# Kernel tuning notes

Hardware: AMD Instinct MI355X
Metric: run time of the kernel (lower is better)

The kernel has to match this reference:

```python
import jax, jax.numpy as jnp
import numpy as np

B, S, D, H, L = 2, 4096, 768, 12, 2
DH = D // H
W = 256            # one-sided sliding window (longformer-base attention_window=512)
VOCAB = 50265
SEP_ID = 2
N_SEPS = 63
G = N_SEPS + 1     # global tokens: <s> at pos 0 + all </s> separators
FF = 4 * D
C = 7
NEG = -1e9


def layer_norm(x, s, b, eps=1e-5):
    m = x.mean(-1, keepdims=True)
    v = ((x - m) ** 2).mean(-1, keepdims=True)
    return (x - m) * jax.lax.rsqrt(v + eps) * s + b


def setup_inputs():
    key = jax.random.key(0)
    keys = iter(jax.random.split(key, 64))
    def nrm(shape, sd=0.02):
        return jax.random.normal(next(keys), shape, jnp.float32) * sd
    input_ids = jax.random.randint(next(keys), (B, S), 5, VOCAB, dtype=jnp.int32)
    input_ids = input_ids.at[:, 0].set(0)  # <s>
    sep_pos = (jnp.arange(N_SEPS) + 1) * (S // (N_SEPS + 1))  # 64,128,...,4032
    input_ids = input_ids.at[:, sep_pos].set(SEP_ID)
    return dict(
        emb_tok=nrm((VOCAB, D)), emb_pos=nrm((S, D)),
        ln_e_s=jnp.ones((D,)), ln_e_b=jnp.zeros((D,)),
        Wq=nrm((L, D, D)), bq=jnp.zeros((L, D)),
        Wk=nrm((L, D, D)), bk=jnp.zeros((L, D)),
        Wv=nrm((L, D, D)), bv=jnp.zeros((L, D)),
        Wqg=nrm((L, D, D)), bqg=jnp.zeros((L, D)),
        Wkg=nrm((L, D, D)), bkg=jnp.zeros((L, D)),
        Wvg=nrm((L, D, D)), bvg=jnp.zeros((L, D)),
        Wo=nrm((L, D, D)), bo=jnp.zeros((L, D)),
        ln1_s=jnp.ones((L, D)), ln1_b=jnp.zeros((L, D)),
        Wf1=nrm((L, D, FF)), bf1=jnp.zeros((L, FF)),
        Wf2=nrm((L, FF, D)), bf2=jnp.zeros((L, D)),
        ln2_s=jnp.ones((L, D)), ln2_b=jnp.zeros((L, D)),
        Wc=nrm((D, C)), bc=jnp.zeros((C,)),
        input_ids=input_ids,
        attention_mask=jnp.ones((B, S), jnp.int32),
        left_overlap=2, right_overlap=2,
    )


def _forward(emb_tok, emb_pos, ln_e_s, ln_e_b, Wq, bq, Wk, bk, Wv, bv,
             Wqg, bqg, Wkg, bkg, Wvg, bvg, Wo, bo, ln1_s, ln1_b,
             Wf1, bf1, Wf2, bf2, ln2_s, ln2_b, Wc, bc,
             input_ids, attention_mask, left_overlap, right_overlap):
    pos = jnp.arange(S)
    # global attention mask: first token + every </s> token (as in the torch forward)
    g_mask = (input_ids == SEP_ID) | (pos[None, :] == 0)                         # [B,S]
    idx_g = jax.vmap(lambda m: jnp.nonzero(m, size=G, fill_value=0)[0])(g_mask)  # [B,G]
    am = attention_mask.astype(jnp.float32)
    key_local_ok = am * (1.0 - g_mask.astype(jnp.float32))  # globals excluded from windowed keys
    nb = S // W
    band_idx = jnp.arange(nb)[:, None] * W + jnp.arange(3 * W)[None, :]  # [nb,3W] into W-padded seq
    rel = jnp.arange(3 * W)[None, :] - W - jnp.arange(W)[:, None]        # key_pos - query_pos
    band_ok = (jnp.abs(rel) <= W)[None, None, None]                       # [1,1,1,W,3W]
    kv_ok = jnp.pad(key_local_ok, ((0, 0), (W, W)))[:, band_idx] > 0      # [B,nb,3W]
    mask = band_ok & kv_ok[:, None, :, None, :]                           # [B,1,nb,W,3W]
    scale = float(DH) ** -0.5
    bix = jnp.arange(B)[:, None]

    x = emb_tok[input_ids] + emb_pos[None]
    x = layer_norm(x, ln_e_s, ln_e_b)
    for l in range(L):
        q = (x @ Wq[l] + bq[l]).reshape(B, S, H, DH)
        k = (x @ Wk[l] + bk[l]).reshape(B, S, H, DH)
        v = (x @ Wv[l] + bv[l]).reshape(B, S, H, DH)
        kb = jnp.pad(k, ((0, 0), (W, W), (0, 0), (0, 0)))[:, band_idx]    # [B,nb,3W,H,DH]
        vb = jnp.pad(v, ((0, 0), (W, W), (0, 0), (0, 0)))[:, band_idx]
        s_band = jnp.einsum('bnqhd,bnkhd->bhnqk', q.reshape(B, nb, W, H, DH), kb) * scale
        s_band = jnp.where(mask, s_band, NEG)
        kg = jnp.take_along_axis(k, idx_g[:, :, None, None], axis=1)      # [B,G,H,DH]
        vg = jnp.take_along_axis(v, idx_g[:, :, None, None], axis=1)
        s_glob = jnp.einsum('bqhd,bghd->bhqg', q, kg) * scale
        probs = jax.nn.softmax(
            jnp.concatenate([s_band.reshape(B, H, S, 3 * W), s_glob], axis=-1), axis=-1)
        out = (jnp.einsum('bhnqk,bnkhd->bnqhd',
                          probs[..., :3 * W].reshape(B, H, nb, W, 3 * W), vb).reshape(B, S, H, DH)
               + jnp.einsum('bhqg,bghd->bqhd', probs[..., 3 * W:], vg)).reshape(B, S, D)
        # global query rows: full attention over all tokens with dedicated global projections
        xg = jnp.take_along_axis(x, idx_g[:, :, None], axis=1)            # [B,G,D]
        qg = (xg @ Wqg[l] + bqg[l]).reshape(B, G, H, DH)
        kga = (x @ Wkg[l] + bkg[l]).reshape(B, S, H, DH)
        vga = (x @ Wvg[l] + bvg[l]).reshape(B, S, H, DH)
        sg = jnp.where(am[:, None, None, :] > 0,
                       jnp.einsum('bghd,bshd->bhgs', qg, kga) * scale, NEG)
        og = jnp.einsum('bhgs,bshd->bghd', jax.nn.softmax(sg, axis=-1), vga).reshape(B, G, D)
        out = out.at[bix, idx_g].set(og)
        x = layer_norm(x + out @ Wo[l] + bo[l], ln1_s[l], ln1_b[l])
        x = layer_norm(x + jax.nn.gelu(x @ Wf1[l] + bf1[l]) @ Wf2[l] + bf2[l], ln2_s[l], ln2_b[l])
    # classification head (eval-mode dropout = identity). Faithful to the torch code,
    # which gathers hidden states at token POSITION j for j in [left, n_seps - right).
    core = x[:, left_overlap:N_SEPS - right_overlap, :]                    # [B, n_core, D]
    return (core @ Wc + bc).reshape(-1, C)


def reference(emb_tok, emb_pos, ln_e_s, ln_e_b, Wq, bq, Wk, bk, Wv, bv,
              Wqg, bqg, Wkg, bkg, Wvg, bvg, Wo, bo, ln1_s, ln1_b,
              Wf1, bf1, Wf2, bf2, ln2_s, ln2_b, Wc, bc,
              input_ids, attention_mask, left_overlap, right_overlap):
    return _forward(emb_tok, emb_pos, ln_e_s, ln_e_b, Wq, bq, Wk, bk, Wv, bv,
                    Wqg, bqg, Wkg, bkg, Wvg, bvg, Wo, bo, ln1_s, ln1_b,
                    Wf1, bf1, Wf2, bf2, ln2_s, ln2_b, Wc, bc,
                    input_ids, attention_mask, left_overlap, right_overlap)
```

## Files before the change

### kernel.cpp

```cpp
#include <hip/hip_runtime.h>
#include <hip/hip_bf16.h>
#include <stdint.h>

#define B_ 2
#define S_ 4096
#define D_ 768
#define H_ 12
#define DH_ 64
#define L_ 2
#define W_ 256
#define G_ 64
#define FF_ 3072
#define C_ 7
#define SEP_ 2
#define NEG_ (-1000000000.0f)
#define NC_ 16

typedef __attribute__((ext_vector_type(8))) short short8;
typedef __attribute__((ext_vector_type(4))) float f32x4;

__device__ __forceinline__ float bfu2f(unsigned short u) {
    return __uint_as_float(((unsigned int)u) << 16);
}
__device__ __forceinline__ unsigned short f2bfu(float f) {
    unsigned int x = __float_as_uint(f);
    unsigned int r = (x + 0x7fffu + ((x >> 16) & 1u)) >> 16;
    return (unsigned short)r;
}
__device__ __forceinline__ float gelu_tanh(float v) {
    float c = 0.7978845608028654f * (v + 0.044715f * v * v * v);
    return 0.5f * v * (1.0f + tanhf(c));
}

__global__ __launch_bounds__(256) void k_wtrans(
    const float* __restrict__ src, unsigned short* __restrict__ dst,
    int K, int N, size_t dstStride) {
    int l = blockIdx.z;
    src += (size_t)l * K * N;
    dst += (size_t)l * dstStride;
    __shared__ unsigned short tile[32][36];
    int t = threadIdx.x;
    int r = t >> 3, c4 = (t & 7) << 2;
    int k0 = blockIdx.y << 5, n0 = blockIdx.x << 5;
    float4 v = *(const float4*)(src + (size_t)(k0 + r) * N + n0 + c4);
    tile[c4 + 0][r] = f2bfu(v.x);
    tile[c4 + 1][r] = f2bfu(v.y);
    tile[c4 + 2][r] = f2bfu(v.z);
    tile[c4 + 3][r] = f2bfu(v.w);
    __syncthreads();
    ushort4 o;
    o.x = tile[r][c4 + 0]; o.y = tile[r][c4 + 1];
    o.z = tile[r][c4 + 2]; o.w = tile[r][c4 + 3];
    *(ushort4*)(dst + (size_t)(n0 + r) * K + k0 + c4) = o;
}

__global__ __launch_bounds__(256) void k_embed_ln(
    const int* __restrict__ ids, const float* __restrict__ etok,
    const float* __restrict__ epos, const float* __restrict__ lns,
    const float* __restrict__ lnb, float* __restrict__ x,
    unsigned short* __restrict__ xb) {
    int row = (blockIdx.x << 2) + (threadIdx.x >> 6);
    int lane = threadIdx.x & 63;
    int s = row & (S_ - 1);
    int id = ids[row];
    const float4* ep = (const float4*)(etok + (size_t)id * D_);
    const float4* pp = (const float4*)(epos + (size_t)s * D_);
    float4 a[3];
    float sum = 0.f, sum2 = 0.f;
#pragma unroll
    for (int i = 0; i < 3; i++) {
        float4 ev = ep[lane + i * 64];
        float4 pv = pp[lane + i * 64];
        ev.x += pv.x; ev.y += pv.y; ev.z += pv.z; ev.w += pv.w;
        a[i] = ev;
        sum  += ev.x + ev.y + ev.z + ev.w;
        sum2 += ev.x * ev.x + ev.y * ev.y + ev.z * ev.z + ev.w * ev.w;
    }
#pragma unroll
    for (int off = 1; off < 64; off <<= 1) {
        sum += __shfl_xor(sum, off);
        sum2 += __shfl_xor(sum2, off);
    }
    float mean = sum * (1.0f / D_);
    float var = sum2 * (1.0f / D_) - mean * mean;
    float rs = rsqrtf(var + 1e-5f);
    float4* xp = (float4*)(x + (size_t)row * D_);
#pragma unroll
    for (int i = 0; i < 3; i++) {
        float4 g = *(const float4*)(lns + lane * 4 + i * 256);
        float4 bb = *(const float4*)(lnb + lane * 4 + i * 256);
        float4 v;
        v.x = (a[i].x - mean) * rs * g.x + bb.x;
        v.y = (a[i].y - mean) * rs * g.y + bb.y;
        v.z = (a[i].z - mean) * rs * g.z + bb.z;
        v.w = (a[i].w - mean) * rs * g.w + bb.w;
        xp[lane + i * 64] = v;
        ushort4 u; u.x = f2bfu(v.x); u.y = f2bfu(v.y); u.z = f2bfu(v.z); u.w = f2bfu(v.w);
        *(ushort4*)(xb + (size_t)row * D_ + lane * 4 + i * 256) = u;
    }
}

__global__ __launch_bounds__(256) void k_add_ln(
    float* __restrict__ x, const float* __restrict__ y, const float* __restrict__ y2,
    const float* __restrict__ lns, const float* __restrict__ lnb,
    unsigned short* __restrict__ xb) {
    int row = (blockIdx.x << 2) + (threadIdx.x >> 6);
    int lane = threadIdx.x & 63;
    float4* xp = (float4*)(x + (size_t)row * D_);
    const float4* yp = (const float4*)(y + (size_t)row * D_);
    const float4* y2p = y2 ? (const float4*)(y2 + (size_t)row * D_) : nullptr;
    float4 a[3];
    float sum = 0.f, sum2 = 0.f;
#pragma unroll
    for (int i = 0; i < 3; i++) {
        float4 xv = xp[lane + i * 64];
        float4 yv = yp[lane + i * 64];
        xv.x += yv.x; xv.y += yv.y; xv.z += yv.z; xv.w += yv.w;
        if (y2p) {
            float4 zv = y2p[lane + i * 64];
            xv.x += zv.x; xv.y += zv.y; xv.z += zv.z; xv.w += zv.w;
        }
        a[i] = xv;
        sum  += xv.x + xv.y + xv.z + xv.w;
        sum2 += xv.x * xv.x + xv.y * xv.y + xv.z * xv.z + xv.w * xv.w;
    }
#pragma unroll
    for (int off = 1; off < 64; off <<= 1) {
        sum += __shfl_xor(sum, off);
        sum2 += __shfl_xor(sum2, off);
    }
    float mean = sum * (1.0f / D_);
    float var = sum2 * (1.0f / D_) - mean * mean;
    float rs = rsqrtf(var + 1e-5f);
#pragma unroll
    for (int i = 0; i < 3; i++) {
        float4 g = *(const float4*)(lns + lane * 4 + i * 256);
        float4 bb = *(const float4*)(lnb + lane * 4 + i * 256);
        float4 v;
        v.x = (a[i].x - mean) * rs * g.x + bb.x;
        v.y = (a[i].y - mean) * rs * g.y + bb.y;
        v.z = (a[i].z - mean) * rs * g.z + bb.z;
        v.w = (a[i].w - mean) * rs * g.w + bb.w;
        xp[lane + i * 64] = v;
        ushort4 u; u.x = f2bfu(v.x); u.y = f2bfu(v.y); u.z = f2bfu(v.z); u.w = f2bfu(v.w);
        *(ushort4*)(xb + (size_t)row * D_ + lane * 4 + i * 256) = u;
    }
}

__global__ __launch_bounds__(256) void k_idx(const int* __restrict__ ids, int* __restrict__ idxg) {
    int b = blockIdx.x;
    int t = threadIdx.x;
    __shared__ int cnt[256];
    __shared__ int totsh;
    int loc[16];
    int n = 0;
#pragma unroll
    for (int i = 0; i < 16; i++) {
        int s = t * 16 + i;
        if (s == 0 || ids[b * S_ + s] == SEP_) loc[n++] = s;
    }
    cnt[t] = n;
    __syncthreads();
    int base = 0;
    for (int u = 0; u < t; u++) base += cnt[u];
    for (int i = 0; i < n; i++) {
        int o = base + i;
        if (o < G_) idxg[b * G_ + o] = loc[i];
    }
    if (t == 255) totsh = base + n;
    __syncthreads();
    if (t == 0)
        for (int o = totsh; o < G_; o++) idxg[b * G_ + o] = 0;
}

__global__ __launch_bounds__(256) void k_gemm_mfma(
    const unsigned short* __restrict__ A, const unsigned short* __restrict__ Wt,
    const float* __restrict__ Wf, const float* __restrict__ bias,
    float* __restrict__ Cf, float* __restrict__ Cf2, unsigned short* __restrict__ Cb,
    int M, int N, int K, int act) {
    __shared__ unsigned short As[128][40];
    __shared__ unsigned short Bs[128][40];
    int t = threadIdx.x;
    int wave = t >> 6, lane = t & 63, l16 = lane & 15, quad = lane >> 4;
    int m0 = blockIdx.y << 7, n0 = blockIdx.x << 7;
    int wm = (wave >> 1) << 6, wn = (wave & 1) << 6;
    int slice = blockIdx.z;
    int kper = K / gridDim.z;
    int kbeg = slice * kper, kend = kbeg + kper;
    f32x4 acc[4][4];
#pragma unroll
    for (int i = 0; i < 4; i++)
#pragma unroll
        for (int j = 0; j < 4; j++) acc[i][j] = (f32x4){0.f, 0.f, 0.f, 0.f};

    int ar = t >> 1, akc = (t & 1) << 4;
    int bn = t & 127, bkh = (t >> 7) << 4;

    for (int k0 = kbeg; k0 < kend; k0 += 32) {
        const unsigned short* ap = A + (size_t)(m0 + ar) * K + k0 + akc;
        *(uint4*)&As[ar][akc] = *(const uint4*)ap;
        *(uint4*)&As[ar][akc + 8] = *(const uint4*)(ap + 8);
        if (Wt) {
            const unsigned short* bp = Wt + (size_t)(n0 + bn) * K + k0 + bkh;
            *(uint4*)&Bs[bn][bkh] = *(const uint4*)bp;
            *(uint4*)&Bs[bn][bkh + 8] = *(const uint4*)(bp + 8);
        } else {
            const float* bp = Wf + (size_t)(k0 + bkh) * N + n0 + bn;
            unsigned int pk[8];
#pragma unroll
            for (int i = 0; i < 8; i++) {
                unsigned int lo = f2bfu(bp[(size_t)(2 * i) * N]);
                unsigned int hi = f2bfu(bp[(size_t)(2 * i + 1) * N]);
                pk[i] = lo | (hi << 16);
            }
            *(uint4*)&Bs[bn][bkh] = *(uint4*)&pk[0];
            *(uint4*)&Bs[bn][bkh + 8] = *(uint4*)&pk[4];
        }
        __syncthreads();
        short8 af[4], bf[4];
#pragma unroll
        for (int i = 0; i < 4; i++) af[i] = *(const short8*)&As[wm + i * 16 + l16][quad * 8];
#pragma unroll
        for (int j = 0; j < 4; j++) bf[j] = *(const short8*)&Bs[wn + j * 16 + l16][quad * 8];
#pragma unroll
        for (int i = 0; i < 4; i++)
#pragma unroll
            for (int j = 0; j < 4; j++)
                acc[i][j] = __builtin_amdgcn_mfma_f32_16x16x32_bf16(af[i], bf[j], acc[i][j], 0, 0, 0);
        __syncthreads();
    }
    float bj[4];
#pragma unroll
    for (int j = 0; j < 4; j++) bj[j] = (slice == 0) ? bias[n0 + wn + j * 16 + l16] : 0.f;
    float* outp = (slice == 0) ? Cf : Cf2;
#pragma unroll
    for (int i = 0; i < 4; i++)
#pragma unroll
        for (int j = 0; j < 4; j++) {
            int col = n0 + wn + j * 16 + l16;
#pragma unroll
            for (int r = 0; r < 4; r++) {
                int row = m0 + wm + i * 16 + quad * 4 + r;
                float v = acc[i][j][r] + bj[j];
                if (act) v = gelu_tanh(v);
                if (outp) outp[(size_t)row * N + col] = v;
                else      Cb[(size_t)row * N + col] = f2bfu(v);
            }
        }
}

struct P5 {
    const unsigned short* Wt[5];
    const float* Wf[5];
    const float* bias[5];
    unsigned short* out[5];
};
__global__ __launch_bounds__(256) void k_gemm_qkv5(
    const unsigned short* __restrict__ A, P5 p) {
    __shared__ unsigned short As[128][40];
    __shared__ unsigned short Bs[128][40];
    const unsigned short* __restrict__ Wt = p.Wt[blockIdx.z];
    const float* __restrict__ Wf = p.Wf[blockIdx.z];
    const float* __restrict__ bias = p.bias[blockIdx.z];
    unsigned short* __restrict__ Cb = p.out[blockIdx.z];
    const int N = D_, K = D_;
    int t = threadIdx.x;
    int wave = t >> 6, lane = t & 63, l16 = lane & 15, quad = lane >> 4;
    int m0 = blockIdx.y << 7, n0 = blockIdx.x << 7;
    int wm = (wave >> 1) << 6, wn = (wave & 1) << 6;
    f32x4 acc[4][4];
#pragma unroll
    for (int i = 0; i < 4; i++)
#pragma unroll
        for (int j = 0; j < 4; j++) acc[i][j] = (f32x4){0.f, 0.f, 0.f, 0.f};

    int ar = t >> 1, akc = (t & 1) << 4;
    int bn = t & 127, bkh = (t >> 7) << 4;

    for (int k0 = 0; k0 < K; k0 += 32) {
        const unsigned short* ap = A + (size_t)(m0 + ar) * K + k0 + akc;
        *(uint4*)&As[ar][akc] = *(const uint4*)ap;
        *(uint4*)&As[ar][akc + 8] = *(const uint4*)(ap + 8);
        if (Wt) {
            const unsigned short* bp = Wt + (size_t)(n0 + bn) * K + k0 + bkh;
            *(uint4*)&Bs[bn][bkh] = *(const uint4*)bp;
            *(uint4*)&Bs[bn][bkh + 8] = *(const uint4*)(bp + 8);
        } else {
            const float* bp = Wf + (size_t)(k0 + bkh) * N + n0 + bn;
            unsigned int pk[8];
#pragma unroll
            for (int i = 0; i < 8; i++) {
                unsigned int lo = f2bfu(bp[(size_t)(2 * i) * N]);
                unsigned int hi = f2bfu(bp[(size_t)(2 * i + 1) * N]);
                pk[i] = lo | (hi << 16);
            }
            *(uint4*)&Bs[bn][bkh] = *(uint4*)&pk[0];
            *(uint4*)&Bs[bn][bkh + 8] = *(uint4*)&pk[4];
        }
        __syncthreads();
        short8 af[4], bf[4];
#pragma unroll
        for (int i = 0; i < 4; i++) af[i] = *(const short8*)&As[wm + i * 16 + l16][quad * 8];
#pragma unroll
        for (int j = 0; j < 4; j++) bf[j] = *(const short8*)&Bs[wn + j * 16 + l16][quad * 8];
#pragma unroll
        for (int i = 0; i < 4; i++)
#pragma unroll
            for (int j = 0; j < 4; j++)
                acc[i][j] = __builtin_amdgcn_mfma_f32_16x16x32_bf16(af[i], bf[j], acc[i][j], 0, 0, 0);
        __syncthreads();
    }
    float bj[4];
#pragma unroll
    for (int j = 0; j < 4; j++) bj[j] = bias[n0 + wn + j * 16 + l16];
#pragma unroll
    for (int i = 0; i < 4; i++)
#pragma unroll
        for (int j = 0; j < 4; j++) {
            int col = n0 + wn + j * 16 + l16;
#pragma unroll
            for (int r = 0; r < 4; r++) {
                int row = m0 + wm + i * 16 + quad * 4 + r;
                float v = acc[i][j][r] + bj[j];
                size_t adr = ((((size_t)(row >> 12)) * H_ + (col >> 6)) * S_ +
                              (row & (S_ - 1))) * DH_ + (col & 63);
                Cb[adr] = f2bfu(v);
            }
        }
}

__global__ __launch_bounds__(256) void k_lattn(
    const unsigned short* __restrict__ q, const unsigned short* __restrict__ k,
    const unsigned short* __restrict__ v, const int* __restrict__ ids,
    const int* __restrict__ am, const int* __restrict__ idxg,
    unsigned short* __restrict__ Tb) {
    int s0 = blockIdx.x << 6, h = blockIdx.y, b = blockIdx.z;
    int t = threadIdx.x;
    int wave = t >> 6, lane = t & 63, l16 = lane & 15, quad = lane >> 4;

    __shared__ unsigned short Ks[64][72];
    __shared__ unsigned short Vt[64][72];
    __shared__ unsigned short Ps[64][72];
    __shared__ unsigned char keyok[64];

    const size_t headbase = (((size_t)b * H_) + h) * S_;
    int qrow = s0 + wave * 16 + l16;
    const unsigned short* qptr = q + (headbase + qrow) * DH_;
    short8 qa0 = *(const short8*)(qptr + quad * 8);
    short8 qa1 = *(const short8*)(qptr + 32 + quad * 8);

    f32x4 O[4];
#pragma unroll
    for (int nf = 0; nf < 4; nf++) O[nf] = (f32x4){0.f, 0.f, 0.f, 0.f};
    float m_run[4] = {-3.4e38f, -3.4e38f, -3.4e38f, -3.4e38f};
    float l_run[4] = {0.f, 0.f, 0.f, 0.f};

    int kbase = s0 - 256;
    int sr = t >> 2, sc = t & 3;

    for (int tile = 0; tile < 10; tile++) {
        int sK, sclamp; bool okf;
        if (tile < 9) {
            sK = kbase + tile * 64 + sr;
            bool inr = (sK >= 0) && (sK < S_);
            sclamp = inr ? sK : 0;
            okf = inr && (am[b * S_ + sclamp] != 0) &&
                  !((ids[b * S_ + sclamp] == SEP_) || (sK == 0));
        } else {
            sK = idxg[b * G_ + sr];
            sclamp = sK; okf = true;
        }
        if (sc == 0) keyok[sr] = okf ? 1 : 0;
        const unsigned short* srcK = k + (headbase + sclamp) * DH_;
        const unsigned short* srcV = v + (headbase + sclamp) * DH_;
        uint4 k0v = *(const uint4*)(srcK + sc * 8);
        uint4 k1v = *(const uint4*)(srcK + (sc + 4) * 8);
        uint4 v0v = *(const uint4*)(srcV + sc * 8);
        uint4 v1v = *(const uint4*)(srcV + (sc + 4) * 8);
        *(uint4*)&Ks[sr][sc * 8] = k0v;
        *(uint4*)&Ks[sr][(sc + 4) * 8] = k1v;
        const unsigned int* vw0 = (const unsigned int*)&v0v;
        const unsigned int* vw1 = (const unsigned int*)&v1v;
#pragma unroll
        for (int i = 0; i < 4; i++) {
            Vt[sc * 8 + 2 * i][sr]      = (unsigned short)(vw0[i] & 0xffff);
            Vt[sc * 8 + 2 * i + 1][sr]  = (unsigned short)(vw0[i] >> 16);
            Vt[(sc + 4) * 8 + 2 * i][sr]     = (unsigned short)(vw1[i] & 0xffff);
            Vt[(sc + 4) * 8 + 2 * i + 1][sr] = (unsigned short)(vw1[i] >> 16);
        }
        __syncthreads();

        f32x4 Sf[4];
#pragma unroll
        for (int nf = 0; nf < 4; nf++) {
            short8 b0 = *(const short8*)&Ks[nf * 16 + l16][quad * 8];
            short8 b1 = *(const short8*)&Ks[nf * 16 + l16][32 + quad * 8];
            f32x4 a = (f32x4){0.f, 0.f, 0.f, 0.f};
            a = __builtin_amdgcn_mfma_f32_16x16x32_bf16(qa0, b0, a, 0, 0, 0);
            a = __builtin_amdgcn_mfma_f32_16x16x32_bf16(qa1, b1, a, 0, 0, 0);
            Sf[nf] = a;
        }
        int ktb = kbase + tile * 64;
        bool kval[4];
#pragma unroll
        for (int nf = 0; nf < 4; nf++) kval[nf] = (tile == 9) || (keyok[nf * 16 + l16] != 0);
        float P_[4][4];
        float mt[4];
#pragma unroll
        for (int r = 0; r < 4; r++) {
            int qs = s0 + wave * 16 + quad * 4 + r;
            float mx = -3.4e38f;
#pragma unroll
            for (int nf = 0; nf < 4; nf++) {
                int ks2 = ktb + nf * 16 + l16;
                bool ok = kval[nf] && ((tile == 9) || (ks2 >= qs - 256 && ks2 <= qs + 256));
                float sv = ok ? Sf[nf][r] * 0.125f : NEG_;
                P_[nf][r] = sv;
                mx = fmaxf(mx, sv);
            }
            mt[r] = mx;
        }
#pragma unroll
        for (int off = 1; off < 16; off <<= 1)
#pragma unroll
            for (int r = 0; r < 4; r++) mt[r] = fmaxf(mt[r], __shfl_xor(mt[r], off));
        float alpha[4], lt[4];
#pragma unroll
        for (int r = 0; r < 4; r++) {
            float mn = fmaxf(m_run[r], mt[r]);
            alpha[r] = __expf(m_run[r] - mn);
            m_run[r] = mn; lt[r] = 0.f;
        }
#pragma unroll
        for (int nf = 0; nf < 4; nf++)
#pragma unroll
            for (int r = 0; r < 4; r++) {
                float p = (P_[nf][r] > -1.0e8f) ? __expf(P_[nf][r] - m_run[r]) : 0.f;
                P_[nf][r] = p; lt[r] += p;
            }
#pragma unroll
        for (int off = 1; off < 16; off <<= 1)
#pragma unroll
            for (int r = 0; r < 4; r++) lt[r] += __shfl_xor(lt[r], off);
#pragma unroll
        for (int r = 0; r < 4; r++) l_run[r] = l_run[r] * alpha[r] + lt[r];
#pragma unroll
        for (int nf = 0; nf < 4; nf++) {
            O[nf][0] *= alpha[0]; O[nf][1] *= alpha[1];
            O[nf][2] *= alpha[2]; O[nf][3] *= alpha[3];
        }
#pragma unroll
        for (int nf = 0; nf < 4; nf++)
#pragma unroll
            for (int r = 0; r < 4; r++)
                Ps[wave * 16 + quad * 4 + r][nf * 16 + l16] = f2bfu(P_[nf][r]);
#pragma unroll
        for (int hh = 0; hh < 2; hh++) {
            short8 pa = *(const short8*)&Ps[wave * 16 + l16][hh * 32 + quad * 8];
#pragma unroll
            for (int nf = 0; nf < 4; nf++) {
                short8 vb8 = *(const short8*)&Vt[nf * 16 + l16][hh * 32 + quad * 8];
                O[nf] = __builtin_amdgcn_mfma_f32_16x16x32_bf16(pa, vb8, O[nf], 0, 0, 0);
            }
        }
        __syncthreads();
    }
#pragma unroll
    for (int r = 0; r < 4; r++) {
        int qs = s0 + wave * 16 + quad * 4 + r;
        float invl = 1.0f / l_run[r];
        size_t base = ((size_t)(b * S_ + qs)) * D_ + h * DH_;
#pragma unroll
        for (int nf = 0; nf < 4; nf++)
            Tb[base + nf * 16 + l16] = f2bfu(O[nf][r] * invl);
    }
}

__global__ __launch_bounds__(256) void k_gattn_part(
    const unsigned short* __restrict__ qg, const unsigned short* __restrict__ kga,
    const unsigned short* __restrict__ vga, const int* __restrict__ am,
    float* __restrict__ Opart, float* __restrict__ mbuf, float* __restrict__ lbuf) {
    int c = blockIdx.x, h = blockIdx.y, b = blockIdx.z;
    int t = threadIdx.x;
    int wave = t >> 6, lane = t & 63, l16 = lane & 15, quad = lane >> 4;

    __shared__ unsigned short Ks[64][72];
    __shared__ unsigned short Vt[64][72];
    __shared__ unsigned short Ps[64][72];
    __shared__ unsigned char keyok[64];

    const size_t headbase = (((size_t)b * H_) + h) * S_;
    int grow = wave * 16 + l16;
    const unsigned short* qptr = qg + ((size_t)(b * G_ + grow)) * D_ + h * DH_;
    short8 qa0 = *(const short8*)(qptr + quad * 8);
    short8 qa1 = *(const short8*)(qptr + 32 + quad * 8);

    f32x4 O[4];
#pragma unroll
    for (int nf = 0; nf < 4; nf++) O[nf] = (f32x4){0.f, 0.f, 0.f, 0.f};
    float m_run[4] = {-3.4e38f, -3.4e38f, -3.4e38f, -3.4e38f};
    float l_run[4] = {0.f, 0.f, 0.f, 0.f};

    int kbase = c * 256;
    int sr = t >> 2, sc = t & 3;

    for (int tile = 0; tile < 4; tile++) {
        int sK = kbase + tile * 64 + sr;
        if (sc == 0) keyok[sr] = (am[b * S_ + sK] != 0) ? 1 : 0;
        const unsigned short* srcK = kga + (headbase + sK) * DH_;
        const unsigned short* srcV = vga + (headbase + sK) * DH_;
        uint4 k0v = *(const uint4*)(srcK + sc * 8);
        uint4 k1v = *(const uint4*)(srcK + (sc + 4) * 8);
        uint4 v0v = *(const uint4*)(srcV + sc * 8);
        uint4 v1v = *(const uint4*)(srcV + (sc + 4) * 8);
        *(uint4*)&Ks[sr][sc * 8] = k0v;
        *(uint4*)&Ks[sr][(sc + 4) * 8] = k1v;
        const unsigned int* vw0 = (const unsigned int*)&v0v;
        const unsigned int* vw1 = (const unsigned int*)&v1v;
#pragma unroll
        for (int i = 0; i < 4; i++) {
            Vt[sc * 8 + 2 * i][sr]      = (unsigned short)(vw0[i] & 0xffff);
            Vt[sc * 8 + 2 * i + 1][sr]  = (unsigned short)(vw0[i] >> 16);
            Vt[(sc + 4) * 8 + 2 * i][sr]     = (unsigned short)(vw1[i] & 0xffff);
            Vt[(sc + 4) * 8 + 2 * i + 1][sr] = (unsigned short)(vw1[i] >> 16);
        }
        __syncthreads();

        f32x4 Sf[4];
#pragma unroll
        for (int nf = 0; nf < 4; nf++) {
            short8 b0 = *(const short8*)&Ks[nf * 16 + l16][quad * 8];
            short8 b1 = *(const short8*)&Ks[nf * 16 + l16][32 + quad * 8];
            f32x4 a = (f32x4){0.f, 0.f, 0.f, 0.f};
            a = __builtin_amdgcn_mfma_f32_16x16x32_bf16(qa0, b0, a, 0, 0, 0);
            a = __builtin_amdgcn_mfma_f32_16x16x32_bf16(qa1, b1, a, 0, 0, 0);
            Sf[nf] = a;
        }
        bool kval[4];
#pragma unroll
        for (int nf = 0; nf < 4; nf++) kval[nf] = (keyok[nf * 16 + l16] != 0);
        float P_[4][4];
        float mt[4];
#pragma unroll
        for (int r = 0; r < 4; r++) {
            float mx = -3.4e38f;
#pragma unroll
            for (int nf = 0; nf < 4; nf++) {
                float sv = kval[nf] ? Sf[nf][r] * 0.125f : NEG_;
                P_[nf][r] = sv;
                mx = fmaxf(mx, sv);
            }
            mt[r] = mx;
        }
#pragma unroll
        for (int off = 1; off < 16; off <<= 1)
#pragma unroll
            for (int r = 0; r < 4; r++) mt[r] = fmaxf(mt[r], __shfl_xor(mt[r], off));
        float alpha[4], lt[4];
#pragma unroll
        for (int r = 0; r < 4; r++) {
            float mn = fmaxf(m_run[r], mt[r]);
            alpha[r] = __expf(m_run[r] - mn);
            m_run[r] = mn; lt[r] = 0.f;
        }
#pragma unroll
        for (int nf = 0; nf < 4; nf++)
#pragma unroll
            for (int r = 0; r < 4; r++) {
                float p = (P_[nf][r] > -1.0e8f) ? __expf(P_[nf][r] - m_run[r]) : 0.f;
                P_[nf][r] = p; lt[r] += p;
            }
#pragma unroll
        for (int off = 1; off < 16; off <<= 1)
#pragma unroll
            for (int r = 0; r < 4; r++) lt[r] += __shfl_xor(lt[r], off);
#pragma unroll
        for (int r = 0; r < 4; r++) l_run[r] = l_run[r] * alpha[r] + lt[r];
#pragma unroll
        for (int nf = 0; nf < 4; nf++) {
            O[nf][0] *= alpha[0]; O[nf][1] *= alpha[1];
            O[nf][2] *= alpha[2]; O[nf][3] *= alpha[3];
        }
#pragma unroll
        for (int nf = 0; nf < 4; nf++)
#pragma unroll
            for (int r = 0; r < 4; r++)
                Ps[wave * 16 + quad * 4 + r][nf * 16 + l16] = f2bfu(P_[nf][r]);
#pragma unroll
        for (int hh = 0; hh < 2; hh++) {
            short8 pa = *(const short8*)&Ps[wave * 16 + l16][hh * 32 + quad * 8];
#pragma unroll
            for (int nf = 0; nf < 4; nf++) {
                short8 vb8 = *(const short8*)&Vt[nf * 16 + l16][hh * 32 + quad * 8];
                O[nf] = __builtin_amdgcn_mfma_f32_16x16x32_bf16(pa, vb8, O[nf], 0, 0, 0);
            }
        }
        __syncthreads();
    }
    size_t bhc = ((size_t)(b * H_ + h)) * NC_ + c;
#pragma unroll
    for (int r = 0; r < 4; r++) {
        int row = wave * 16 + quad * 4 + r;
#pragma unroll
        for (int nf = 0; nf < 4; nf++)
            Opart[bhc * (G_ * DH_) + (size_t)row * DH_ + nf * 16 + l16] = O[nf][r];
        if (l16 == 0) {
            mbuf[bhc * G_ + row] = m_run[r];
            lbuf[bhc * G_ + row] = l_run[r];
        }
    }
}

__global__ __launch_bounds__(64) void k_gattn_comb(
    const float* __restrict__ Opart, const float* __restrict__ mbuf,
    const float* __restrict__ lbuf, const int* __restrict__ idxg,
    unsigned short* __restrict__ Tb) {
    int g = blockIdx.x, h = blockIdx.y, b = blockIdx.z;
    int d = threadIdx.x;
    size_t bh = (size_t)(b * H_ + h);
    float M = -3.4e38f;
    float mv[NC_];
#pragma unroll
    for (int c = 0; c < NC_; c++) {
        mv[c] = mbuf[(bh * NC_ + c) * G_ + g];
        M = fmaxf(M, mv[c]);
    }
    float L = 0.f, o = 0.f;
#pragma unroll
    for (int c = 0; c < NC_; c++) {
        float e = __expf(mv[c] - M);
        L += lbuf[(bh * NC_ + c) * G_ + g] * e;
        o += Opart[(bh * NC_ + c) * (G_ * DH_) + (size_t)g * DH_ + d] * e;
    }
    int srow = idxg[b * G_ + g];
    Tb[((size_t)(b * S_ + srow)) * D_ + h * DH_ + d] = f2bfu(o / L);
}

__global__ __launch_bounds__(256) void k_gemm(
    const float* __restrict__ A, const float* __restrict__ Bw,
    const float* __restrict__ bias, float* __restrict__ Cf,
    unsigned short* __restrict__ Cb, int M, int N, int K, int act) {
    __shared__ float As[16][68];
    __shared__ float Bs[16][68];
    int tl = threadIdx.x;
    int tx = tl & 15, ty = tl >> 4;
    int m0 = blockIdx.y << 6, n0 = blockIdx.x << 6;
    float c[4][4] = {{0.f}};
    int arow = tl >> 2, akk = (tl & 3) << 2;
    int bkk = tl >> 4, bcol = (tl & 15) << 2;
    for (int k0 = 0; k0 < K; k0 += 16) {
        float4 a4 = *(const float4*)(A + (size_t)(m0 + arow) * K + k0 + akk);
        As[akk + 0][arow] = a4.x; As[akk + 1][arow] = a4.y;
        As[akk + 2][arow] = a4.z; As[akk + 3][arow] = a4.w;
        float4 b4 = *(const float4*)(Bw + (size_t)(k0 + bkk) * N + n0 + bcol);
        Bs[bkk][bcol + 0] = b4.x; Bs[bkk][bcol + 1] = b4.y;
        Bs[bkk][bcol + 2] = b4.z; Bs[bkk][bcol + 3] = b4.w;
        __syncthreads();
#pragma unroll
        for (int kk = 0; kk < 16; kk++) {
            float4 av = *(const float4*)&As[kk][ty << 2];
            float4 bv = *(const float4*)&Bs[kk][tx << 2];
            float aa[4] = {av.x, av.y, av.z, av.w};
            float bb[4] = {bv.x, bv.y, bv.z, bv.w};
#pragma unroll
            for (int i = 0; i < 4; i++)
#pragma unroll
                for (int j = 0; j < 4; j++) c[i][j] += aa[i] * bb[j];
        }
        __syncthreads();
    }
    float bias4[4];
#pragma unroll
    for (int j = 0; j < 4; j++) bias4[j] = bias[n0 + (tx << 2) + j];
#pragma unroll
    for (int i = 0; i < 4; i++) {
        int mrow = m0 + (ty << 2) + i;
        float v0 = c[i][0] + bias4[0], v1 = c[i][1] + bias4[1];
        float v2 = c[i][2] + bias4[2], v3 = c[i][3] + bias4[3];
        if (act) { v0 = gelu_tanh(v0); v1 = gelu_tanh(v1); v2 = gelu_tanh(v2); v3 = gelu_tanh(v3); }
        if (Cf) {
            float4 o; o.x = v0; o.y = v1; o.z = v2; o.w = v3;
            *(float4*)(Cf + (size_t)mrow * N + n0 + (tx << 2)) = o;
        } else {
            ushort4 o; o.x = f2bfu(v0); o.y = f2bfu(v1); o.z = f2bfu(v2); o.w = f2bfu(v3);
            *(ushort4*)(Cb + (size_t)mrow * N + n0 + (tx << 2)) = o;
        }
    }
}

__global__ __launch_bounds__(256) void k_gather_xg(
    const float* __restrict__ x, const int* __restrict__ idxg, float* __restrict__ xg) {
    int bg = blockIdx.x;
    int b = bg / G_;
    int srow = idxg[bg];
    for (int d = threadIdx.x; d < D_; d += 256)
        xg[(size_t)bg * D_ + d] = x[((size_t)(b * S_ + srow)) * D_ + d];
}

__global__ __launch_bounds__(256) void k_classifier(
    const float* __restrict__ x, const float* __restrict__ Wc,
    const float* __restrict__ bc, const int* __restrict__ lo_p,
    int rows_pb, float* __restrict__ out) {
    int r = blockIdx.x;
    int b = r / rows_pb, i = r % rows_pb;
    int s = lo_p[0] + i;
    int t = threadIdx.x;
    __shared__ float xr[D_];
    __shared__ float red[256];
    const float* xrow = x + ((size_t)(b * S_ + s)) * D_;
    for (int d = t; d < D_; d += 256) xr[d] = xrow[d];
    __syncthreads();
    for (int c = 0; c < C_; c++) {
        float loc = 0.f;
        for (int d = t; d < D_; d += 256) loc += xr[d] * Wc[d * C_ + c];
        red[t] = loc; __syncthreads();
        for (int o = 128; o; o >>= 1) { if (t < o) red[t] += red[t + o]; __syncthreads(); }
        if (t == 0) out[r * C_ + c] = red[0] + bc[c];
        __syncthreads();
    }
}

extern "C" void kernel_launch(void* const* d_in, const int* in_sizes, int n_in,
                              void* d_out, int out_size, void* d_ws, size_t ws_size,
                              hipStream_t stream) {
    (void)in_sizes; (void)n_in;
    const float* emb_tok = (const float*)d_in[0];
    const float* emb_pos = (const float*)d_in[1];
    const float* ln_e_s = (const float*)d_in[2];
    const float* ln_e_b = (const float*)d_in[3];
    const float* Wq  = (const float*)d_in[4];
    const float* bq  = (const float*)d_in[5];
    const float* Wk  = (const float*)d_in[6];
    const float* bk  = (const float*)d_in[7];
    const float* Wv  = (const float*)d_in[8];
    const float* bv  = (const float*)d_in[9];
    const float* Wqg = (const float*)d_in[10];
    const float* bqg = (const float*)d_in[11];
    const float* Wkg = (const float*)d_in[12];
    const float* bkg = (const float*)d_in[13];
    const float* Wvg = (const float*)d_in[14];
    const float* bvg = (const float*)d_in[15];
    const float* Wo  = (const float*)d_in[16];
    const float* bo  = (const float*)d_in[17];
    const float* ln1_s = (const float*)d_in[18];
    const float* ln1_b = (const float*)d_in[19];
    const float* Wf1 = (const float*)d_in[20];
    const float* bf1 = (const float*)d_in[21];
    const float* Wf2 = (const float*)d_in[22];
    const float* bf2 = (const float*)d_in[23];
    const float* ln2_s = (const float*)d_in[24];
    const float* ln2_b = (const float*)d_in[25];
    const float* Wc  = (const float*)d_in[26];
    const float* bc  = (const float*)d_in[27];
    const int* input_ids = (const int*)d_in[28];
    const int* attn_mask = (const int*)d_in[29];
    const int* lo        = (const int*)d_in[30];

    const size_t SZB = (size_t)B_ * S_ * D_;
    const size_t D2 = (size_t)D_ * D_;
    const size_t PL = 6 * D2 + 2 * (size_t)D_ * FF_;
    uint8_t* w = (uint8_t*)d_ws;
    float*          x    = (float*)w;
    unsigned short* xb   = (unsigned short*)(w + 4 * SZB);
    float*          P    = (float*)(w + 6 * SZB);
    unsigned short* qb   = (unsigned short*)(w + 10 * SZB);
    unsigned short* kb   = (unsigned short*)(w + 12 * SZB);
    unsigned short* vb   = (unsigned short*)(w + 14 * SZB);
    unsigned short* kgab = (unsigned short*)(w + 16 * SZB);
    unsigned short* vgab = (unsigned short*)(w + 18 * SZB);
    unsigned short* Hb   = (unsigned short*)(w + 10 * SZB);
    unsigned short* Tb   = (unsigned short*)(w + 20 * SZB);
    float* xg = (float*)(w + 22 * SZB);
    unsigned short* qgb = (unsigned short*)(w + 22 * SZB + (size_t)B_ * G_ * D_ * 4);
    int* idxg = (int*)(w + 22 * SZB + (size_t)B_ * G_ * D_ * 4 + (size_t)B_ * G_ * D_ * 2);
    float* Opart = (float*)(w + 23 * SZB);
    float* mbuf  = (float*)(w + 24 * SZB);
    float* lbuf  = mbuf + (size_t)B_ * H_ * NC_ * G_;

    const size_t P2_OFF = 24 * SZB + (1u << 20);
    const size_t WB_OFF = P2_OFF + 4 * SZB;
    const size_t NEED_P2 = WB_OFF;
    const size_t NEED_W = WB_OFF + L_ * PL * 2;
    float* P2 = (float*)(w + P2_OFF);
    unsigned short* wb = (unsigned short*)(w + WB_OFF);
    const int useW = (ws_size >= NEED_W) ? 1 : 0;
    const int useSplit = (ws_size >= NEED_P2) ? 1 : 0;

    const int BS = B_ * S_;

    if (useW) {
        k_wtrans<<<dim3(D_/32, D_/32, L_), 256, 0, stream>>>(Wq,  wb + 0*D2, D_, D_, PL);
        k_wtrans<<<dim3(D_/32, D_/32, L_), 256, 0, stream>>>(Wk,  wb + 1*D2, D_, D_, PL);
        k_wtrans<<<dim3(D_/32, D_/32, L_), 256, 0, stream>>>(Wv,  wb + 2*D2, D_, D_, PL);
        k_wtrans<<<dim3(D_/32, D_/32, L_), 256, 0, stream>>>(Wkg, wb + 3*D2, D_, D_, PL);
        k_wtrans<<<dim3(D_/32, D_/32, L_), 256, 0, stream>>>(Wvg, wb + 4*D2, D_, D_, PL);
        k_wtrans<<<dim3(D_/32, D_/32, L_), 256, 0, stream>>>(Wo,  wb + 5*D2, D_, D_, PL);
        k_wtrans<<<dim3(FF_/32, D_/32, L_), 256, 0, stream>>>(Wf1, wb + 6*D2, D_, FF_, PL);
        k_wtrans<<<dim3(D_/32, FF_/32, L_), 256, 0, stream>>>(Wf2, wb + 6*D2 + (size_t)D_*FF_, FF_, D_, PL);
    }

    k_embed_ln<<<BS / 4, 256, 0, stream>>>(input_ids, emb_tok, emb_pos, ln_e_s, ln_e_b, x, xb);
    k_idx<<<B_, 256, 0, stream>>>(input_ids, idxg);

    dim3 g_d(D_ / 128, BS / 128);
    dim3 g_ds(D_ / 128, BS / 128, useSplit ? 2 : 1);
    dim3 g_d5(D_ / 128, BS / 128, 5);
    dim3 g_ff(FF_ / 128, BS / 128);
    dim3 g_qg(D_ / 64, (B_ * G_) / 64);

    for (int l = 0; l < L_; l++) {
        const unsigned short* wbl = wb + (size_t)l * PL;
        P5 p5;
        p5.Wf[0] = Wq  + (size_t)l * D2;  p5.bias[0] = bq  + l * D_;  p5.out[0] = qb;
        p5.Wf[1] = Wk  + (size_t)l * D2;  p5.bias[1] = bk  + l * D_;  p5.out[1] = kb;
        p5.Wf[2] = Wv  + (size_t)l * D2;  p5.bias[2] = bv  + l * D_;  p5.out[2] = vb;
        p5.Wf[3] = Wkg + (size_t)l * D2;  p5.bias[3] = bkg + l * D_;  p5.out[3] = kgab;
        p5.Wf[4] = Wvg + (size_t)l * D2;  p5.bias[4] = bvg + l * D_;  p5.out[4] = vgab;
        for (int i = 0; i < 5; i++) p5.Wt[i] = useW ? (wbl + (size_t)i * D2) : nullptr;
        const float* Wqg_l = Wqg + (size_t)l * D2;
        const float* Wo_l  = Wo  + (size_t)l * D2;
        const float* Wf1_l = Wf1 + (size_t)l * D_ * FF_;
        const float* Wf2_l = Wf2 + (size_t)l * FF_ * D_;
        const unsigned short* Wo_t  = useW ? (wbl + 5 * D2) : nullptr;
        const unsigned short* Wf1_t = useW ? (wbl + 6 * D2) : nullptr;
        const unsigned short* Wf2_t = useW ? (wbl + 6 * D2 + (size_t)D_ * FF_) : nullptr;

        k_gemm_qkv5<<<g_d5, 256, 0, stream>>>(xb, p5);
        k_lattn<<<dim3(S_ / 64, H_, B_), 256, 0, stream>>>(qb, kb, vb, input_ids, attn_mask, idxg, Tb);
        k_gather_xg<<<B_ * G_, 256, 0, stream>>>(x, idxg, xg);
        k_gemm<<<g_qg, 256, 0, stream>>>(xg, Wqg_l, bqg + l * D_, nullptr, qgb, B_ * G_, D_, D_, 0);
        k_gattn_part<<<dim3(NC_, H_, B_), 256, 0, stream>>>(qgb, kgab, vgab, attn_mask, Opart, mbuf, lbuf);
        k_gattn_comb<<<dim3(G_, H_, B_), 64, 0, stream>>>(Opart, mbuf, lbuf, idxg, Tb);
        k_gemm_mfma<<<g_ds, 256, 0, stream>>>(Tb, Wo_t, Wo_l, bo + l * D_, P, P2, nullptr, BS, D_, D_, 0);
        k_add_ln<<<BS / 4, 256, 0, stream>>>(x, P, useSplit ? P2 : nullptr, ln1_s + l * D_, ln1_b + l * D_, xb);
        k_gemm_mfma<<<g_ff, 256, 0, stream>>>(xb, Wf1_t, Wf1_l, bf1 + l * FF_, nullptr, nullptr, Hb, BS, FF_, D_, 1);
        k_gemm_mfma<<<g_ds, 256, 0, stream>>>(Hb, Wf2_t, Wf2_l, bf2 + l * D_, P, P2, nullptr, BS, D_, FF_, 0);
        k_add_ln<<<BS / 4, 256, 0, stream>>>(x, P, useSplit ? P2 : nullptr, ln2_s + l * D_, ln2_b + l * D_, xb);
    }

    int rows = out_size / C_;
    int rows_pb = rows / B_;
    k_classifier<<<rows, 256, 0, stream>>>(x, Wc, bc, lo, rows_pb, (float*)d_out);
}
```

Baseline: 1.277 ms.

## Load GEMM tiles directly into LDS and remap blocks across XCDs

```diff
diff --git a/kernel.cpp b/kernel.cpp
--- a/kernel.cpp
+++ b/kernel.cpp
@@ -31,6 +31,43 @@
     float c = 0.7978845608028654f * (v + 0.044715f * v * v * v);
     return 0.5f * v * (1.0f + tanhf(c));
 }
+
+__device__ __forceinline__ void gl16(const unsigned short* g, unsigned short* l) {
+    __builtin_amdgcn_global_load_lds(
+        (const __attribute__((address_space(1))) unsigned int*)g,
+        (__attribute__((address_space(3))) unsigned int*)l,
+        16, 0, 0);
+}
+
+__device__ __forceinline__ void xcd_remap(int& bx, int& by, int& bz) {
+    int nx = gridDim.x, ny = gridDim.y, nz = gridDim.z;
+    int flat = bx + nx * (by + ny * bz);
+    int nxz = nx * nz;
+    int xcd = flat & 7;
+    int n = flat >> 3;
+    int band = n / nxz;
+    int r = n - band * nxz;
+    by = xcd * (ny >> 3) + band;
+    bz = r / nx;
+    bx = r - bz * nx;
+}
+
+#define GEMM_COMPUTE()                                                                   \
+    {                                                                                    \
+        short8 af[4], bf[4];                                                             \
+        _Pragma("unroll")                                                                \
+        for (int i_ = 0; i_ < 4; i_++)                                                   \
+            af[i_] = *(const short8*)&As[(wm + i_ * 16 + l16) * 32 + quad * 8];          \
+        _Pragma("unroll")                                                                \
+        for (int j_ = 0; j_ < 4; j_++)                                                   \
+            bf[j_] = *(const short8*)&Bs[(wn + j_ * 16 + l16) * 32 + quad * 8];          \
+        _Pragma("unroll")                                                                \
+        for (int i_ = 0; i_ < 4; i_++)                                                   \
+            _Pragma("unroll")                                                            \
+            for (int j_ = 0; j_ < 4; j_++)                                               \
+                acc[i_][j_] = __builtin_amdgcn_mfma_f32_16x16x32_bf16(af[i_], bf[j_],    \
+                                                                      acc[i_][j_], 0, 0, 0); \
+    }
 
 __global__ __launch_bounds__(256) void k_wtrans(
     const float* __restrict__ src, unsigned short* __restrict__ dst,
@@ -178,13 +215,15 @@
     const float* __restrict__ Wf, const float* __restrict__ bias,
     float* __restrict__ Cf, float* __restrict__ Cf2, unsigned short* __restrict__ Cb,
     int M, int N, int K, int act) {
-    __shared__ unsigned short As[128][40];
-    __shared__ unsigned short Bs[128][40];
+    __shared__ __align__(16) unsigned short As[128 * 32];
+    __shared__ __align__(16) unsigned short Bs[128 * 32];
+    int bx = blockIdx.x, by = blockIdx.y, bz = blockIdx.z;
+    xcd_remap(bx, by, bz);
     int t = threadIdx.x;
     int wave = t >> 6, lane = t & 63, l16 = lane & 15, quad = lane >> 4;
-    int m0 = blockIdx.y << 7, n0 = blockIdx.x << 7;
+    int m0 = by << 7, n0 = bx << 7;
     int wm = (wave >> 1) << 6, wn = (wave & 1) << 6;
-    int slice = blockIdx.z;
+    int slice = bz;
     int kper = K / gridDim.z;
     int kbeg = slice * kper, kend = kbeg + kper;
     f32x4 acc[4][4];
@@ -193,18 +232,31 @@
 #pragma unroll
         for (int j = 0; j < 4; j++) acc[i][j] = (f32x4){0.f, 0.f, 0.f, 0.f};
 
-    int ar = t >> 1, akc = (t & 1) << 4;
-    int bn = t & 127, bkh = (t >> 7) << 4;
-
-    for (int k0 = kbeg; k0 < kend; k0 += 32) {
-        const unsigned short* ap = A + (size_t)(m0 + ar) * K + k0 + akc;
-        *(uint4*)&As[ar][akc] = *(const uint4*)ap;
-        *(uint4*)&As[ar][akc + 8] = *(const uint4*)(ap + 8);
-        if (Wt) {
-            const unsigned short* bp = Wt + (size_t)(n0 + bn) * K + k0 + bkh;
-            *(uint4*)&Bs[bn][bkh] = *(const uint4*)bp;
-            *(uint4*)&Bs[bn][bkh + 8] = *(const uint4*)(bp + 8);
-        } else {
+    int ch = wave * 128 + lane;
+    int srow = ch >> 2, spos = ch & 3;
+    unsigned short* al0 = As + wave * 1024;
+    unsigned short* al1 = As + wave * 1024 + 512;
+    unsigned short* bl0 = Bs + wave * 1024;
+    unsigned short* bl1 = Bs + wave * 1024 + 512;
+    const unsigned short* ag = A + (size_t)(m0 + srow) * K + kbeg + spos * 8;
+
+    if (Wt) {
+        const unsigned short* bg = Wt + (size_t)(n0 + srow) * K + kbeg + spos * 8;
+        for (int k0 = kbeg; k0 < kend; k0 += 32) {
+            gl16(ag, al0);
+            gl16(ag + (size_t)16 * K, al1);
+            gl16(bg, bl0);
+            gl16(bg + (size_t)16 * K, bl1);
+            __syncthreads();
+            GEMM_COMPUTE();
+            __syncthreads();
+            ag += 32; bg += 32;
+        }
+    } else {
+        int bn = t & 127, bkh = (t >> 7) << 4;
+        for (int k0 = kbeg; k0 < kend; k0 += 32) {
+            gl16(ag, al0);
+            gl16(ag + (size_t)16 * K, al1);
             const float* bp = Wf + (size_t)(k0 + bkh) * N + n0 + bn;
             unsigned int pk[8];
 #pragma unroll
@@ -213,21 +265,13 @@
                 unsigned int hi = f2bfu(bp[(size_t)(2 * i + 1) * N]);
                 pk[i] = lo | (hi << 16);
             }
-            *(uint4*)&Bs[bn][bkh] = *(uint4*)&pk[0];
-            *(uint4*)&Bs[bn][bkh + 8] = *(uint4*)&pk[4];
-        }
-        __syncthreads();
-        short8 af[4], bf[4];
-#pragma unroll
-        for (int i = 0; i < 4; i++) af[i] = *(const short8*)&As[wm + i * 16 + l16][quad * 8];
-#pragma unroll
-        for (int j = 0; j < 4; j++) bf[j] = *(const short8*)&Bs[wn + j * 16 + l16][quad * 8];
-#pragma unroll
-        for (int i = 0; i < 4; i++)
-#pragma unroll
-            for (int j = 0; j < 4; j++)
-                acc[i][j] = __builtin_amdgcn_mfma_f32_16x16x32_bf16(af[i], bf[j], acc[i][j], 0, 0, 0);
-        __syncthreads();
+            *(uint4*)&Bs[bn * 32 + bkh] = *(uint4*)&pk[0];
+            *(uint4*)&Bs[bn * 32 + bkh + 8] = *(uint4*)&pk[4];
+            __syncthreads();
+            GEMM_COMPUTE();
+            __syncthreads();
+            ag += 32;
+        }
     }
     float bj[4];
 #pragma unroll
@@ -257,16 +301,18 @@
 };
 __global__ __launch_bounds__(256) void k_gemm_qkv5(
     const unsigned short* __restrict__ A, P5 p) {
-    __shared__ unsigned short As[128][40];
-    __shared__ unsigned short Bs[128][40];
-    const unsigned short* __restrict__ Wt = p.Wt[blockIdx.z];
-    const float* __restrict__ Wf = p.Wf[blockIdx.z];
-    const float* __restrict__ bias = p.bias[blockIdx.z];
-    unsigned short* __restrict__ Cb = p.out[blockIdx.z];
+    __shared__ __align__(16) unsigned short As[128 * 32];
+    __shared__ __align__(16) unsigned short Bs[128 * 32];
+    int bx = blockIdx.x, by = blockIdx.y, bz = blockIdx.z;
+    xcd_remap(bx, by, bz);
+    const unsigned short* __restrict__ Wt = p.Wt[bz];
+    const float* __restrict__ Wf = p.Wf[bz];
+    const float* __restrict__ bias = p.bias[bz];
+    unsigned short* __restrict__ Cb = p.out[bz];
     const int N = D_, K = D_;
     int t = threadIdx.x;
     int wave = t >> 6, lane = t & 63, l16 = lane & 15, quad = lane >> 4;
-    int m0 = blockIdx.y << 7, n0 = blockIdx.x << 7;
+    int m0 = by << 7, n0 = bx << 7;
     int wm = (wave >> 1) << 6, wn = (wave & 1) << 6;
     f32x4 acc[4][4];
 #pragma unroll
@@ -274,18 +320,30 @@
 #pragma unroll
         for (int j = 0; j < 4; j++) acc[i][j] = (f32x4){0.f, 0.f, 0.f, 0.f};
 
-    int ar = t >> 1, akc = (t & 1) << 4;
-    int bn = t & 127, bkh = (t >> 7) << 4;
-
-    for (int k0 = 0; k0 < K; k0 += 32) {
-        const unsigned short* ap = A + (size_t)(m0 + ar) * K + k0 + akc;
-        *(uint4*)&As[ar][akc] = *(const uint4*)ap;
-        *(uint4*)&As[ar][akc + 8] = *(const uint4*)(ap + 8);
-        if (Wt) {
-            const unsigned short* bp = Wt + (size_t)(n0 + bn) * K + k0 + bkh;
-            *(uint4*)&Bs[bn][bkh] = *(const uint4*)bp;
-            *(uint4*)&Bs[bn][bkh + 8] = *(const uint4*)(bp + 8);
-        } else {
+    int ch = wave * 128 + lane;
+    int srow = ch >> 2, spos = ch & 3;
+    unsigned short* al0 = As + wave * 1024;
+    unsigned short* al1 = As + wave * 1024 + 512;
+    unsigned short* bl0 = Bs + wave * 1024;
+    unsigned short* bl1 = Bs + wave * 1024 + 512;
+    const unsigned short* ag = A + (size_t)(m0 + srow) * K + spos * 8;
+
+    if (Wt) {
+        const unsigned short* bg = Wt + (size_t)(n0 + srow) * K + spos * 8;
+        for (int k0 = 0; k0 < K; k0 += 32) {
+            gl16(ag + k0, al0);
+            gl16(ag + 16 * K + k0, al1);
+            gl16(bg + k0, bl0);
+            gl16(bg + 16 * K + k0, bl1);
+            __syncthreads();
+            GEMM_COMPUTE();
+            __syncthreads();
+        }
+    } else {
+        int bn = t & 127, bkh = (t >> 7) << 4;
+        for (int k0 = 0; k0 < K; k0 += 32) {
+            gl16(ag + k0, al0);
+            gl16(ag + 16 * K + k0, al1);
             const float* bp = Wf + (size_t)(k0 + bkh) * N + n0 + bn;
             unsigned int pk[8];
 #pragma unroll
@@ -294,21 +352,12 @@
                 unsigned int hi = f2bfu(bp[(size_t)(2 * i + 1) * N]);
                 pk[i] = lo | (hi << 16);
             }
-            *(uint4*)&Bs[bn][bkh] = *(uint4*)&pk[0];
-            *(uint4*)&Bs[bn][bkh + 8] = *(uint4*)&pk[4];
-        }
-        __syncthreads();
-        short8 af[4], bf[4];
-#pragma unroll
-        for (int i = 0; i < 4; i++) af[i] = *(const short8*)&As[wm + i * 16 + l16][quad * 8];
-#pragma unroll
-        for (int j = 0; j < 4; j++) bf[j] = *(const short8*)&Bs[wn + j * 16 + l16][quad * 8];
-#pragma unroll
-        for (int i = 0; i < 4; i++)
-#pragma unroll
-            for (int j = 0; j < 4; j++)
-                acc[i][j] = __builtin_amdgcn_mfma_f32_16x16x32_bf16(af[i], bf[j], acc[i][j], 0, 0, 0);
-        __syncthreads();
+            *(uint4*)&Bs[bn * 32 + bkh] = *(uint4*)&pk[0];
+            *(uint4*)&Bs[bn * 32 + bkh + 8] = *(uint4*)&pk[4];
+            __syncthreads();
+            GEMM_COMPUTE();
+            __syncthreads();
+        }
     }
     float bj[4];
 #pragma unroll
```

Result: faster. 1.160 ms (-9.2%).
